# Optimization experiments

Measured on AMD Instinct MI355X. Metric: run time of the kernel, lower is better.

The kernel has to match this reference:

```python
import jax, jax.numpy as jnp
import numpy as np
from jax import lax

N = 4096          # n_nodes
D_IN = 64         # node_attr_size
H = 64            # hidden_size
MAX_ITER = 10


def setup_inputs() -> dict:
    key = jax.random.key(0)
    ks = jax.random.split(key, 6)
    # Scale L and recurrent weights so the tanh fixed-point iteration is well-behaved
    X = jax.random.normal(ks[0], (N, D_IN), dtype=jnp.float32)
    L = jax.random.normal(ks[1], (N, N), dtype=jnp.float32) / jnp.sqrt(jnp.float32(N))
    W_ih0 = jax.random.normal(ks[2], (H, D_IN), dtype=jnp.float32) * 0.5
    W_hh0 = jax.random.normal(ks[3], (H, H), dtype=jnp.float32) * 0.5
    W_ih1 = jax.random.normal(ks[4], (H, H), dtype=jnp.float32) * 0.5
    W_hh1 = jax.random.normal(ks[5], (H, H), dtype=jnp.float32) * 0.5
    return {"X": X, "L": L, "W_ih0": W_ih0, "W_hh0": W_hh0,
            "W_ih1": W_ih1, "W_hh1": W_hh1}


def _gesn_layer(x, L, W_ih, W_hh):
    # wiu = linear(X, W_ih) computed once; then iterate
    # h <- tanh(wiu + L @ (h @ W_hh^T)) for max_iter steps (fixed-count
    # version of the torch convergence loop; see notes).
    wiu = x @ W_ih.T                                   # [N, H]
    h0 = jnp.zeros((x.shape[0], W_hh.shape[0]), x.dtype)

    def step(h, _):
        z = wiu + L @ (h @ W_hh.T)                     # [N, H]
        return jnp.tanh(z), None

    h, _ = lax.scan(step, h0, None, length=MAX_ITER)
    return h


def reference(X, L, W_ih0, W_hh0, W_ih1, W_hh1):
    h1 = _gesn_layer(X, L, W_ih0, W_hh0)               # layer 0: [N, H]
    h2 = _gesn_layer(h1, L, W_ih1, W_hh1)              # layer 1: [N, H]
    return jnp.concatenate([h1, h2], axis=-1)          # [N, 2H]
```

## Files before the change

### kernel.cpp

```cpp
#include <hip/hip_runtime.h>
#include <hip/hip_bf16.h>
#include <math.h>


#define NN 4096
#define HH 64

typedef float  f32x4  __attribute__((ext_vector_type(4)));
typedef short  bf16x8 __attribute__((ext_vector_type(8)));

static __device__ __forceinline__ unsigned short bf16_bits(__hip_bfloat16 b) {
    union { __hip_bfloat16 b; unsigned short u; } cv; cv.b = b; return cv.u;
}

__global__ __launch_bounds__(256) void convert_L(
    const float* __restrict__ L, short* __restrict__ Ahi, short* __restrict__ Alo)
{
    __shared__ float T[16 * 132];
    const int t  = threadIdx.x;
    const int rb = blockIdx.x >> 5;
    const int kg = blockIdx.x & 31;

    {
        const int row = t >> 4;
        const int c4  = (t & 15) * 4;
        const float* src = L + (size_t)(rb * 16 + row) * NN + kg * 128;
        float4 v0 = *reinterpret_cast<const float4*>(src + c4);
        float4 v1 = *reinterpret_cast<const float4*>(src + c4 + 64);
        *reinterpret_cast<float4*>(&T[row * 132 + c4])      = v0;
        *reinterpret_cast<float4*>(&T[row * 132 + c4 + 64]) = v1;
    }
    __syncthreads();

    const int kbl = t >> 6;
    const int l   = t & 63;
    const int r   = l & 15, g = l >> 4;
    short hi8[8], lo8[8];
#pragma unroll
    for (int j = 0; j < 8; ++j) {
        const float v = T[r * 132 + kbl * 32 + g * 8 + j];
        __hip_bfloat16 bh = __float2bfloat16(v);
        const float vh = __bfloat162float(bh);
        __hip_bfloat16 bl = __float2bfloat16(v - vh);
        hi8[j] = (short)bf16_bits(bh);
        lo8[j] = (short)bf16_bits(bl);
    }
    const size_t off = ((size_t)(rb * 128 + kg * 4 + kbl) * 64 + l) * 8;
    *reinterpret_cast<bf16x8*>(Ahi + off) = *reinterpret_cast<bf16x8*>(hi8);
    *reinterpret_cast<bf16x8*>(Alo + off) = *reinterpret_cast<bf16x8*>(lo8);
}

__global__ __launch_bounds__(256) void gesn_mm(
    const short* __restrict__ Ahi, const short* __restrict__ Alo,
    const short* __restrict__ Bhi, const short* __restrict__ Blo,
    float* __restrict__ Gp)
{
    __shared__ short Bh_lds[16 * 4 * 64 * 8];
    __shared__ short Bl_lds[16 * 4 * 64 * 8];

    const int t = threadIdx.x;
    const int w = t >> 6, l = t & 63;
    const int p = blockIdx.x >> 3;
    const int s = blockIdx.x & 7;
    const int rb0 = p * 8 + w * 2;
    const int kb0 = s * 16;

    {
        const short* srcH = Bhi + (size_t)kb0 * 4 * 64 * 8;
        const short* srcL = Blo + (size_t)kb0 * 4 * 64 * 8;
#pragma unroll
        for (int q = 0; q < 16; ++q) {
            const int idx = (q * 256 + t) * 8;
            *reinterpret_cast<bf16x8*>(&Bh_lds[idx]) =
                *reinterpret_cast<const bf16x8*>(srcH + idx);
            *reinterpret_cast<bf16x8*>(&Bl_lds[idx]) =
                *reinterpret_cast<const bf16x8*>(srcL + idx);
        }
    }
    __syncthreads();

    const size_t abase0 = ((size_t)((rb0 + 0) * 128 + kb0) * 64 + l) * 8;
    const size_t abase1 = ((size_t)((rb0 + 1) * 128 + kb0) * 64 + l) * 8;

    bf16x8 aH[4][2], aL[4][2];
#pragma unroll
    for (int q = 0; q < 3; ++q) {
        aH[q][0] = *reinterpret_cast<const bf16x8*>(Ahi + abase0 + (size_t)q * 512);
        aL[q][0] = *reinterpret_cast<const bf16x8*>(Alo + abase0 + (size_t)q * 512);
        aH[q][1] = *reinterpret_cast<const bf16x8*>(Ahi + abase1 + (size_t)q * 512);
        aL[q][1] = *reinterpret_cast<const bf16x8*>(Alo + abase1 + (size_t)q * 512);
    }

    f32x4 acc[2][4] = {};

#pragma unroll
    for (int kbl = 0; kbl < 16; ++kbl) {
        const int cur = kbl & 3;
        if (kbl + 3 < 16) {
            const int nxt = (kbl + 3) & 3;
            aH[nxt][0] = *reinterpret_cast<const bf16x8*>(Ahi + abase0 + (size_t)(kbl + 3) * 512);
            aL[nxt][0] = *reinterpret_cast<const bf16x8*>(Alo + abase0 + (size_t)(kbl + 3) * 512);
            aH[nxt][1] = *reinterpret_cast<const bf16x8*>(Ahi + abase1 + (size_t)(kbl + 3) * 512);
            aL[nxt][1] = *reinterpret_cast<const bf16x8*>(Alo + abase1 + (size_t)(kbl + 3) * 512);
        }
        bf16x8 bH[4], bL[4];
#pragma unroll
        for (int cf = 0; cf < 4; ++cf) {
            const int idx = ((kbl * 4 + cf) * 64 + l) * 8;
            bH[cf] = *reinterpret_cast<const bf16x8*>(&Bh_lds[idx]);
            bL[cf] = *reinterpret_cast<const bf16x8*>(&Bl_lds[idx]);
        }
#pragma unroll
        for (int rf = 0; rf < 2; ++rf)
#pragma unroll
            for (int cf = 0; cf < 4; ++cf) {
                acc[rf][cf] = __builtin_amdgcn_mfma_f32_16x16x32_bf16(
                    aH[cur][rf], bH[cf], acc[rf][cf], 0, 0, 0);
                acc[rf][cf] = __builtin_amdgcn_mfma_f32_16x16x32_bf16(
                    aH[cur][rf], bL[cf], acc[rf][cf], 0, 0, 0);
                acc[rf][cf] = __builtin_amdgcn_mfma_f32_16x16x32_bf16(
                    aL[cur][rf], bH[cf], acc[rf][cf], 0, 0, 0);
            }
    }

    float* g = Gp + (size_t)s * NN * HH;
    const int col0  = l & 15;
    const int rbase = (l >> 4) * 4;
#pragma unroll
    for (int rf = 0; rf < 2; ++rf)
#pragma unroll
        for (int cf = 0; cf < 4; ++cf)
#pragma unroll
            for (int r = 0; r < 4; ++r)
                g[(size_t)((rb0 + rf) * 16 + rbase + r) * HH + cf * 16 + col0]
                    = acc[rf][cf][r];
}

__global__ __launch_bounds__(256) void gesn_post(
    const float* __restrict__ Gsrc, int nsplit,
    const float* __restrict__ wiu_in, float* __restrict__ wiu_out,
    const float* __restrict__ W,
    float* __restrict__ hf32,
    short* __restrict__ Bhi, short* __restrict__ Blo,
    float* __restrict__ out2, int outc0)
{
    __shared__ float W_lds[64 * 65];
    __shared__ float G_lds[16 * 68];
    __shared__ unsigned short Hi_lds[16][66];
    __shared__ unsigned short Lo_lds[16][66];
    const int t = threadIdx.x;

    {
        const int j  = t >> 2;
        const int k0 = (t & 3) << 4;
#pragma unroll
        for (int q = 0; q < 16; ++q)
            W_lds[j * 65 + k0 + q] = W[j * 64 + k0 + q];
    }
    const int r0 = blockIdx.x * 16;

    {
        const int row = t >> 4;
        const int c4  = (t & 15) * 4;
        float4 sum;
        if (nsplit == 0) {
            sum = *reinterpret_cast<const float4*>(
                Gsrc + (size_t)(r0 + row) * HH + c4);
        } else {
            sum = make_float4(0.f, 0.f, 0.f, 0.f);
            for (int sidx = 0; sidx < nsplit; ++sidx) {
                const float4 v = *reinterpret_cast<const float4*>(
                    Gsrc + (size_t)sidx * NN * HH + (size_t)(r0 + row) * HH + c4);
                sum.x += v.x; sum.y += v.y; sum.z += v.z; sum.w += v.w;
            }
        }
        *reinterpret_cast<float4*>(&G_lds[row * 68 + c4]) = sum;
    }
    __syncthreads();

    const int j  = t & 63;
    const int ig = t >> 6;
#pragma unroll
    for (int rr = 0; rr < 4; ++rr) {
        const int i = ig * 4 + rr;
        float z = wiu_in ? wiu_in[(size_t)(r0 + i) * HH + j] : 0.f;
#pragma unroll
        for (int m = 0; m < 64; ++m)
            z = fmaf(G_lds[i * 68 + m], W_lds[j * 65 + m], z);
        if (wiu_out) wiu_out[(size_t)(r0 + i) * HH + j] = z;
        const float hv = tanhf(z);
        hf32[(size_t)(r0 + i) * HH + j] = hv;
        if (out2) out2[(size_t)(r0 + i) * 128 + outc0 + j] = hv;
        __hip_bfloat16 bh = __float2bfloat16(hv);
        const float vh = __bfloat162float(bh);
        __hip_bfloat16 bl = __float2bfloat16(hv - vh);
        Hi_lds[i][j] = bf16_bits(bh);
        Lo_lds[i][j] = bf16_bits(bl);
    }
    __syncthreads();

    if (t < 128) {
        const int j2     = t & 63;
        const int glocal = t >> 6;
        const int kb     = r0 >> 5;
        const int gg     = ((r0 & 31) >> 3) + glocal;
        const int cf     = j2 >> 4;
        const int lane   = gg * 16 + (j2 & 15);
        short hi8[8], lo8[8];
#pragma unroll
        for (int jj = 0; jj < 8; ++jj) {
            const int i = glocal * 8 + jj;
            hi8[jj] = (short)Hi_lds[i][j2];
            lo8[jj] = (short)Lo_lds[i][j2];
        }
        const size_t off = ((size_t)(kb * 4 + cf) * 64 + lane) * 8;
        *reinterpret_cast<bf16x8*>(Bhi + off) = *reinterpret_cast<bf16x8*>(hi8);
        *reinterpret_cast<bf16x8*>(Blo + off) = *reinterpret_cast<bf16x8*>(lo8);
    }
}

__global__ __launch_bounds__(256) void gesn_input_kernel(
    const float* __restrict__ x, const float* __restrict__ W,
    float* __restrict__ wiu, float* __restrict__ h)
{
    __shared__ float W_lds[64 * 65];
    __shared__ float x_lds[256];
    const int t = threadIdx.x;
    {
        const int j  = t >> 2;
        const int k0 = (t & 3) << 4;
#pragma unroll
        for (int q = 0; q < 16; ++q)
            W_lds[j * 65 + k0 + q] = W[j * 64 + k0 + q];
    }
    const int i0 = blockIdx.x * 4;
    x_lds[t] = x[i0 * 64 + t];
    __syncthreads();
    const int j = t & 63, i = t >> 6;
    float z = 0.f;
#pragma unroll
    for (int k = 0; k < 64; ++k)
        z = fmaf(x_lds[i * 64 + k], W_lds[j * 65 + k], z);
    const int gidx = (i0 + i) * 64 + j;
    wiu[gidx] = z;
    h[gidx]   = tanhf(z);
}

__global__ __launch_bounds__(256) void gesn_iter_kernel(
    const float* __restrict__ L, const float* __restrict__ h_in,
    const float* __restrict__ wiu, const float* __restrict__ W,
    float* __restrict__ h_out, float* __restrict__ out2, int out_col0)
{
    __shared__ float h_lds[64 * 64];
    __shared__ float L_lds[16 * 68];
    __shared__ float G_lds[16 * 68];
    __shared__ float W_lds[64 * 65];
    const int t = threadIdx.x;
    {
        const int j  = t >> 2;
        const int k0 = (t & 3) << 4;
#pragma unroll
        for (int q = 0; q < 16; ++q)
            W_lds[j * 65 + k0 + q] = W[j * 64 + k0 + q];
    }
    const int r0 = blockIdx.x * 16;
    const int p  = t >> 5;
    const int c0 = (t & 31) * 2;
    float acc00 = 0.f, acc01 = 0.f, acc10 = 0.f, acc11 = 0.f;
    const int lr = t >> 4;
    const int lc = (t & 15) * 4;
    for (int kb = 0; kb < 64; ++kb) {
        __syncthreads();
        const float4 lv = *reinterpret_cast<const float4*>(
            &L[(size_t)(r0 + lr) * 4096 + kb * 64 + lc]);
        *reinterpret_cast<float4*>(&L_lds[lr * 68 + lc]) = lv;
        const float4* hsrc = reinterpret_cast<const float4*>(h_in + kb * 4096);
        float4* hdst = reinterpret_cast<float4*>(h_lds);
#pragma unroll
        for (int q = 0; q < 4; ++q)
            hdst[t + 256 * q] = hsrc[t + 256 * q];
        __syncthreads();
#pragma unroll
        for (int kk = 0; kk < 64; ++kk) {
            const float  lv0 = L_lds[(2 * p) * 68 + kk];
            const float  lv1 = L_lds[(2 * p + 1) * 68 + kk];
            const float2 hv  = *reinterpret_cast<const float2*>(&h_lds[kk * 64 + c0]);
            acc00 = fmaf(lv0, hv.x, acc00);
            acc01 = fmaf(lv0, hv.y, acc01);
            acc10 = fmaf(lv1, hv.x, acc10);
            acc11 = fmaf(lv1, hv.y, acc11);
        }
    }
    G_lds[(2 * p) * 68 + c0]         = acc00;
    G_lds[(2 * p) * 68 + c0 + 1]     = acc01;
    G_lds[(2 * p + 1) * 68 + c0]     = acc10;
    G_lds[(2 * p + 1) * 68 + c0 + 1] = acc11;
    __syncthreads();
    const int j  = t & 63;
    const int iw = t >> 6;
#pragma unroll
    for (int rr = 0; rr < 4; ++rr) {
        const int i = iw * 4 + rr;
        float z = wiu[(size_t)(r0 + i) * 64 + j];
#pragma unroll
        for (int m = 0; m < 64; ++m)
            z = fmaf(G_lds[i * 68 + m], W_lds[j * 65 + m], z);
        const float hv = tanhf(z);
        h_out[(size_t)(r0 + i) * 64 + j] = hv;
        if (out2) out2[(size_t)(r0 + i) * 128 + out_col0 + j] = hv;
    }
}

extern "C" void kernel_launch(void* const* d_in, const int* in_sizes, int n_in,
                              void* d_out, int out_size, void* d_ws, size_t ws_size,
                              hipStream_t stream) {
    const float* X    = (const float*)d_in[0];
    const float* L    = (const float*)d_in[1];
    const float* Wih0 = (const float*)d_in[2];
    const float* Whh0 = (const float*)d_in[3];
    const float* Wih1 = (const float*)d_in[4];
    const float* Whh1 = (const float*)d_in[5];
    float* out = (float*)d_out;
    char* ws = (char*)d_ws;

    const size_t MB = 1024 * 1024;
    const size_t need = 76 * MB;

    if (ws_size >= need) {
        short* Ahi = (short*)(ws);
        short* Alo = (short*)(ws + 32 * MB);
        short* Bhi = (short*)(ws + 64 * MB);
        short* Blo = (short*)(ws + 64 * MB + 512 * 1024);
        float* wiu = (float*)(ws + 65 * MB);
        float* hA  = (float*)(ws + 66 * MB);
        float* hB  = (float*)(ws + 67 * MB);
        float* Gp  = (float*)(ws + 68 * MB);

        convert_L<<<8192, 256, 0, stream>>>(L, Ahi, Alo);

        for (int layer = 0; layer < 2; ++layer) {
            const float* x   = layer ? hA : X;
            const float* Wih = layer ? Wih1 : Wih0;
            const float* Whh = layer ? Whh1 : Whh0;
            float* hcur = layer ? hB : hA;

            gesn_post<<<256, 256, 0, stream>>>(x, 0, nullptr, wiu, Wih,
                                               hcur, Bhi, Blo, nullptr, 0);
            for (int it = 0; it < 9; ++it) {
                gesn_mm<<<256, 256, 0, stream>>>(Ahi, Alo, Bhi, Blo, Gp);
                float* o2 = (it == 8) ? out : nullptr;
                gesn_post<<<256, 256, 0, stream>>>(Gp, 8, wiu, nullptr, Whh,
                                                   hcur, Bhi, Blo, o2, layer * 64);
            }
        }
    } else {
        float* wiu = (float*)(ws);
        float* hA  = (float*)(ws + (1u << 20));
        float* hB  = (float*)(ws + (2u << 20));
        for (int layer = 0; layer < 2; ++layer) {
            const float* x   = layer ? hB : X;
            const float* Wih = layer ? Wih1 : Wih0;
            const float* Whh = layer ? Whh1 : Whh0;
            gesn_input_kernel<<<1024, 256, 0, stream>>>(x, Wih, wiu, hA);
            float* cur = hA;
            float* nxt = hB;
            for (int it = 0; it < 9; ++it) {
                float* o2 = (it == 8) ? out : nullptr;
                gesn_iter_kernel<<<256, 256, 0, stream>>>(L, cur, wiu, Whh, nxt,
                                                          o2, layer * 64);
                float* tmp = cur; cur = nxt; nxt = tmp;
            }
        }
    }
}
```

Before: 529.7 us.

## Use 8 waves per block with one row tile each and split accumulators

The matmul kernel now runs 512 threads per block, with each wave owning one 16-row tile instead of two. The B tile is shared across twice as many waves, which doubles the number of waves available to hide memory latency. The hi*hi products and the correction terms go into separate accumulators, so consecutive MFMAs no longer depend on each other. The cost is fewer A-tile registers reused per wave, plus an extra add when the result is written out.

```diff
diff --git a/kernel.cpp b/kernel.cpp
--- a/kernel.cpp
+++ b/kernel.cpp
@@ -50,7 +50,7 @@
     *reinterpret_cast<bf16x8*>(Alo + off) = *reinterpret_cast<bf16x8*>(lo8);
 }
 
-__global__ __launch_bounds__(256) void gesn_mm(
+__global__ __launch_bounds__(512) void gesn_mm(
     const short* __restrict__ Ahi, const short* __restrict__ Alo,
     const short* __restrict__ Bhi, const short* __restrict__ Blo,
     float* __restrict__ Gp)
@@ -62,15 +62,15 @@
     const int w = t >> 6, l = t & 63;
     const int p = blockIdx.x >> 3;
     const int s = blockIdx.x & 7;
-    const int rb0 = p * 8 + w * 2;
+    const int rb = p * 8 + w;
     const int kb0 = s * 16;
 
     {
         const short* srcH = Bhi + (size_t)kb0 * 4 * 64 * 8;
         const short* srcL = Blo + (size_t)kb0 * 4 * 64 * 8;
 #pragma unroll
-        for (int q = 0; q < 16; ++q) {
-            const int idx = (q * 256 + t) * 8;
+        for (int q = 0; q < 8; ++q) {
+            const int idx = (q * 512 + t) * 8;
             *reinterpret_cast<bf16x8*>(&Bh_lds[idx]) =
                 *reinterpret_cast<const bf16x8*>(srcH + idx);
             *reinterpret_cast<bf16x8*>(&Bl_lds[idx]) =
@@ -79,29 +79,25 @@
     }
     __syncthreads();
 
-    const size_t abase0 = ((size_t)((rb0 + 0) * 128 + kb0) * 64 + l) * 8;
-    const size_t abase1 = ((size_t)((rb0 + 1) * 128 + kb0) * 64 + l) * 8;
-
-    bf16x8 aH[4][2], aL[4][2];
+    const size_t abase = ((size_t)(rb * 128 + kb0) * 64 + l) * 8;
+
+    bf16x8 aH[4], aL[4];
 #pragma unroll
     for (int q = 0; q < 3; ++q) {
-        aH[q][0] = *reinterpret_cast<const bf16x8*>(Ahi + abase0 + (size_t)q * 512);
-        aL[q][0] = *reinterpret_cast<const bf16x8*>(Alo + abase0 + (size_t)q * 512);
-        aH[q][1] = *reinterpret_cast<const bf16x8*>(Ahi + abase1 + (size_t)q * 512);
-        aL[q][1] = *reinterpret_cast<const bf16x8*>(Alo + abase1 + (size_t)q * 512);
-    }
-
-    f32x4 acc[2][4] = {};
+        aH[q] = *reinterpret_cast<const bf16x8*>(Ahi + abase + (size_t)q * 512);
+        aL[q] = *reinterpret_cast<const bf16x8*>(Alo + abase + (size_t)q * 512);
+    }
+
+    f32x4 accP[4] = {};
+    f32x4 accQ[4] = {};
 
 #pragma unroll
     for (int kbl = 0; kbl < 16; ++kbl) {
         const int cur = kbl & 3;
         if (kbl + 3 < 16) {
             const int nxt = (kbl + 3) & 3;
-            aH[nxt][0] = *reinterpret_cast<const bf16x8*>(Ahi + abase0 + (size_t)(kbl + 3) * 512);
-            aL[nxt][0] = *reinterpret_cast<const bf16x8*>(Alo + abase0 + (size_t)(kbl + 3) * 512);
-            aH[nxt][1] = *reinterpret_cast<const bf16x8*>(Ahi + abase1 + (size_t)(kbl + 3) * 512);
-            aL[nxt][1] = *reinterpret_cast<const bf16x8*>(Alo + abase1 + (size_t)(kbl + 3) * 512);
+            aH[nxt] = *reinterpret_cast<const bf16x8*>(Ahi + abase + (size_t)(kbl + 3) * 512);
+            aL[nxt] = *reinterpret_cast<const bf16x8*>(Alo + abase + (size_t)(kbl + 3) * 512);
         }
         bf16x8 bH[4], bL[4];
 #pragma unroll
@@ -111,29 +107,25 @@
             bL[cf] = *reinterpret_cast<const bf16x8*>(&Bl_lds[idx]);
         }
 #pragma unroll
-        for (int rf = 0; rf < 2; ++rf)
-#pragma unroll
-            for (int cf = 0; cf < 4; ++cf) {
-                acc[rf][cf] = __builtin_amdgcn_mfma_f32_16x16x32_bf16(
-                    aH[cur][rf], bH[cf], acc[rf][cf], 0, 0, 0);
-                acc[rf][cf] = __builtin_amdgcn_mfma_f32_16x16x32_bf16(
-                    aH[cur][rf], bL[cf], acc[rf][cf], 0, 0, 0);
-                acc[rf][cf] = __builtin_amdgcn_mfma_f32_16x16x32_bf16(
-                    aL[cur][rf], bH[cf], acc[rf][cf], 0, 0, 0);
-            }
+        for (int cf = 0; cf < 4; ++cf) {
+            accP[cf] = __builtin_amdgcn_mfma_f32_16x16x32_bf16(
+                aH[cur], bH[cf], accP[cf], 0, 0, 0);
+            accQ[cf] = __builtin_amdgcn_mfma_f32_16x16x32_bf16(
+                aH[cur], bL[cf], accQ[cf], 0, 0, 0);
+            accQ[cf] = __builtin_amdgcn_mfma_f32_16x16x32_bf16(
+                aL[cur], bH[cf], accQ[cf], 0, 0, 0);
+        }
     }
 
     float* g = Gp + (size_t)s * NN * HH;
     const int col0  = l & 15;
     const int rbase = (l >> 4) * 4;
 #pragma unroll
-    for (int rf = 0; rf < 2; ++rf)
-#pragma unroll
-        for (int cf = 0; cf < 4; ++cf)
-#pragma unroll
-            for (int r = 0; r < 4; ++r)
-                g[(size_t)((rb0 + rf) * 16 + rbase + r) * HH + cf * 16 + col0]
-                    = acc[rf][cf][r];
+    for (int cf = 0; cf < 4; ++cf)
+#pragma unroll
+        for (int r = 0; r < 4; ++r)
+            g[(size_t)(rb * 16 + rbase + r) * HH + cf * 16 + col0]
+                = accP[cf][r] + accQ[cf][r];
 }
 
 __global__ __launch_bounds__(256) void gesn_post(
@@ -347,7 +339,7 @@
             gesn_post<<<256, 256, 0, stream>>>(x, 0, nullptr, wiu, Wih,
                                                hcur, Bhi, Blo, nullptr, 0);
             for (int it = 0; it < 9; ++it) {
-                gesn_mm<<<256, 256, 0, stream>>>(Ahi, Alo, Bhi, Blo, Gp);
+                gesn_mm<<<256, 512, 0, stream>>>(Ahi, Alo, Bhi, Blo, Gp);
                 float* o2 = (it == 8) ? out : nullptr;
                 gesn_post<<<256, 256, 0, stream>>>(Gp, 8, wiu, nullptr, Whh,
                                                    hcur, Bhi, Blo, o2, layer * 64);
```

Measured after the change: 516.8 us. 2.4% less time.
